# Kernel tuning notes

Hardware: AMD Instinct MI355X
Metric: run time of the kernel (lower is better)

Reference implementation:

```python
import jax, jax.numpy as jnp
import numpy as np

N_PIXELS = 262144
N_CENTERS = 1024
N_G = 256

def setup_inputs() -> dict:
    key = jax.random.key(0)
    k1, k2, k3, k4, k5 = jax.random.split(key, 5)
    return {
        "alphas": jax.random.normal(k1, (N_CENTERS, 1), dtype=jnp.float32),
        "betas": jax.random.normal(k2, (N_G, 2), dtype=jnp.float32) * 0.1,
        "K": jax.random.normal(k3, (N_PIXELS, N_G), dtype=jnp.float32) * 0.05,
        "all_pixels": jax.random.normal(k4, (N_PIXELS, 2), dtype=jnp.float32),
        "all_p_centers": jax.random.normal(k5, (N_CENTERS, 2), dtype=jnp.float32),
        "sdp2": jnp.ones((), dtype=jnp.float32) * 2.0,
    }

def reference(alphas, betas, K, all_pixels, all_p_centers, sdp2):
    # deformed pixel coordinates: (n_pixels, 2)
    deformed = all_pixels - K @ betas
    # pairwise squared distances via norm expansion (same math as the torch
    # ones-matmul broadcasting, expressed with plain broadcasting):
    p_norm2 = jnp.sum(jnp.square(deformed), axis=1, keepdims=True)      # (n_pixels, 1)
    c_norm2 = jnp.sum(jnp.square(all_p_centers), axis=1)                # (n_centers,)
    p_dot_c = 2.0 * (deformed @ all_p_centers.T)                        # (n_pixels, n_centers)
    big_matrix = p_norm2 + c_norm2[None, :] - p_dot_c
    kBp = jnp.exp(-big_matrix / (2.0 * sdp2))
    return kBp @ alphas                                                  # (n_pixels, 1)
```

## Files before the change

kernel.cpp:

```cpp
#include <hip/hip_runtime.h>

#if defined(__has_builtin)
#  if __has_builtin(__builtin_amdgcn_exp2f)
#    define EXP2F(x) __builtin_amdgcn_exp2f(x)
#  else
#    define EXP2F(x) exp2f(x)
#  endif
#else
#  define EXP2F(x) exp2f(x)
#endif

constexpr int NPIX  = 262144;
constexpr int NC    = 1024;
constexpr int NG    = 256;
constexpr int BLOCK = 256;
constexpr int GRID  = NPIX / 512;

template <int CTRL>
__device__ __forceinline__ float dpp_add(float v) {
    union { float f; int i; } u, t;
    u.f = v;
    t.i = __builtin_amdgcn_update_dpp(0, u.i, CTRL, 0xF, 0xF, true);
    return v + t.f;
}
template <int CTRL>
__device__ __forceinline__ float dpp_mov(float v) {
    union { float f; int i; } u, t;
    u.f = v;
    t.i = __builtin_amdgcn_update_dpp(0, u.i, CTRL, 0xF, 0xF, true);
    return t.f;
}
__device__ __forceinline__ float sum64_lane63(float v) {
    v = dpp_add<0xB1>(v);
    v = dpp_add<0x4E>(v);
    v = dpp_add<0x141>(v);
    v = dpp_add<0x140>(v);
    v = dpp_add<0x142>(v);
    v = dpp_add<0x143>(v);
    return v;
}
__device__ __forceinline__ float readlane63(float v) {
    union { float f; int i; } u; u.f = v;
    union { int i; float f; } r;
    r.i = __builtin_amdgcn_readlane(u.i, 63);
    return r.f;
}

__global__ __launch_bounds__(BLOCK, 4)
void kbpa_pipe(const float* __restrict__ alphas,
               const float* __restrict__ betas,
               const float* __restrict__ K,
               const float* __restrict__ pixels,
               const float* __restrict__ centers,
               const float* __restrict__ sdp2p,
               float* __restrict__ out)
{
    const int lane = threadIdx.x & 63;
    const int wave = threadIdx.x >> 6;

    const float f   = -1.44269504088896340736f / (2.0f * sdp2p[0]);
    const float m2f = -2.0f * f;

    float4 rcx[4], rcy[4], rca[4];
    {
        const float4* c4 = (const float4*)centers;
        const float4* a4 = (const float4*)alphas;
        #pragma unroll
        for (int j = 0; j < 4; ++j) {
            const float4 p0 = c4[lane * 8 + 2 * j];
            const float4 p1 = c4[lane * 8 + 2 * j + 1];
            rcx[j] = make_float4(p0.x, p0.z, p1.x, p1.z);
            rcy[j] = make_float4(p0.y, p0.w, p1.y, p1.w);
            const float4 al = a4[lane * 4 + j];
            rca[j].x = al.x * EXP2F(f * (rcx[j].x * rcx[j].x + rcy[j].x * rcy[j].x));
            rca[j].y = al.y * EXP2F(f * (rcx[j].y * rcx[j].y + rcy[j].y * rcy[j].y));
            rca[j].z = al.z * EXP2F(f * (rcx[j].z * rcx[j].z + rcy[j].z * rcy[j].z));
            rca[j].w = al.w * EXP2F(f * (rcx[j].w * rcx[j].w + rcy[j].w * rcy[j].w));
        }
    }

    const float4* bf4 = (const float4*)betas;
    const float4 bb0 = bf4[2 * lane];
    const float4 bb1 = bf4[2 * lane + 1];

    const int w0 = blockIdx.x * 512 + wave * 128;
    const float2 px0 = ((const float2*)pixels)[w0 + lane];
    const float2 px1 = ((const float2*)pixels)[w0 + 64 + lane];

    float dx0 = 0.f, dy0 = 0.f;
    #pragma unroll 1
    for (int g = 0; g < 16; ++g) {
        float4 kv[4];
        #pragma unroll
        for (int j = 0; j < 4; ++j)
            kv[j] = ((const float4*)(K + (size_t)(w0 + g * 4 + j) * NG))[lane];
        #pragma unroll
        for (int j = 0; j < 4; ++j) {
            float sx = kv[j].x * bb0.x + kv[j].y * bb0.z;
            float sy = kv[j].x * bb0.y + kv[j].y * bb0.w;
            sx = fmaf(kv[j].z, bb1.x, sx); sy = fmaf(kv[j].z, bb1.y, sy);
            sx = fmaf(kv[j].w, bb1.z, sx); sy = fmaf(kv[j].w, bb1.w, sy);
            sx = sum64_lane63(sx); sy = sum64_lane63(sy);
            const float tx = readlane63(sx);
            const float ty = readlane63(sy);
            if (lane == g * 4 + j) { dx0 = px0.x - tx; dy0 = px0.y - ty; }
        }
    }

    float dxs = m2f * dx0, dys = m2f * dy0, acc = 0.f;
    float dx1 = 0.f, dy1 = 0.f;
    #pragma unroll 1
    for (int g = 0; g < 16; ++g) {
        float4 kv[4];
        #pragma unroll
        for (int j = 0; j < 4; ++j)
            kv[j] = ((const float4*)(K + (size_t)(w0 + 64 + g * 4 + j) * NG))[lane];

        #pragma unroll
        for (int t = 0; t < 4; ++t) {
            float t0 = 0.f, t1 = 0.f, t2 = 0.f, t3 = 0.f;
            #pragma unroll
            for (int j = 0; j < 4; ++j) {
                t0 = fmaf(rca[j].x, EXP2F(fmaf(dxs, rcx[j].x, dys * rcy[j].x)), t0);
                t1 = fmaf(rca[j].y, EXP2F(fmaf(dxs, rcx[j].y, dys * rcy[j].y)), t1);
                t2 = fmaf(rca[j].z, EXP2F(fmaf(dxs, rcx[j].z, dys * rcy[j].z)), t2);
                t3 = fmaf(rca[j].w, EXP2F(fmaf(dxs, rcx[j].w, dys * rcy[j].w)), t3);
            }
            acc += (t0 + t1) + (t2 + t3);
            dxs = dpp_mov<0x121>(dxs);
            dys = dpp_mov<0x121>(dys);
            acc = dpp_mov<0x121>(acc);
        }
        if ((g & 3) == 3) {
            const int sw = lane ^ (((g >> 2) & 1) ? 32 : 16);
            dxs = __shfl(dxs, sw);
            dys = __shfl(dys, sw);
            acc = __shfl(acc, sw);
        }

        #pragma unroll
        for (int j = 0; j < 4; ++j) {
            float sx = kv[j].x * bb0.x + kv[j].y * bb0.z;
            float sy = kv[j].x * bb0.y + kv[j].y * bb0.w;
            sx = fmaf(kv[j].z, bb1.x, sx); sy = fmaf(kv[j].z, bb1.y, sy);
            sx = fmaf(kv[j].w, bb1.z, sx); sy = fmaf(kv[j].w, bb1.w, sy);
            sx = sum64_lane63(sx); sy = sum64_lane63(sy);
            const float tx = readlane63(sx);
            const float ty = readlane63(sy);
            if (lane == g * 4 + j) { dx1 = px1.x - tx; dy1 = px1.y - ty; }
        }
    }
    out[w0 + lane] = acc * EXP2F(f * (dx0 * dx0 + dy0 * dy0));

    float dxs1 = m2f * dx1, dys1 = m2f * dy1, acc1 = 0.f;
    #pragma unroll 1
    for (int round = 0; round < 4; ++round) {
        #pragma unroll 2
        for (int t = 0; t < 16; ++t) {
            float t0 = 0.f, t1 = 0.f, t2 = 0.f, t3 = 0.f;
            #pragma unroll
            for (int j = 0; j < 4; ++j) {
                t0 = fmaf(rca[j].x, EXP2F(fmaf(dxs1, rcx[j].x, dys1 * rcy[j].x)), t0);
                t1 = fmaf(rca[j].y, EXP2F(fmaf(dxs1, rcx[j].y, dys1 * rcy[j].y)), t1);
                t2 = fmaf(rca[j].z, EXP2F(fmaf(dxs1, rcx[j].z, dys1 * rcy[j].z)), t2);
                t3 = fmaf(rca[j].w, EXP2F(fmaf(dxs1, rcx[j].w, dys1 * rcy[j].w)), t3);
            }
            acc1 += (t0 + t1) + (t2 + t3);
            dxs1 = dpp_mov<0x121>(dxs1);
            dys1 = dpp_mov<0x121>(dys1);
            acc1 = dpp_mov<0x121>(acc1);
        }
        const int sw = lane ^ ((round & 1) ? 32 : 16);
        dxs1 = __shfl(dxs1, sw);
        dys1 = __shfl(dys1, sw);
        acc1 = __shfl(acc1, sw);
    }
    out[w0 + 64 + lane] = acc1 * EXP2F(f * (dx1 * dx1 + dy1 * dy1));
}

extern "C" void kernel_launch(void* const* d_in, const int* in_sizes, int n_in,
                              void* d_out, int out_size, void* d_ws, size_t ws_size,
                              hipStream_t stream)
{
    const float* alphas  = (const float*)d_in[0];
    const float* betas   = (const float*)d_in[1];
    const float* K       = (const float*)d_in[2];
    const float* pixels  = (const float*)d_in[3];
    const float* centers = (const float*)d_in[4];
    const float* sdp2    = (const float*)d_in[5];
    float* outp          = (float*)d_out;

    hipLaunchKernelGGL(kbpa_pipe, dim3(GRID), dim3(BLOCK), 0, stream,
                       alphas, betas, K, pixels, centers, sdp2, outp);
}
```

Measured before the change: 76.94 us.

## Double-buffer K row loads and remap block order across XCDs

K rows are now loaded into two alternating register buffers, so the next group's global loads are in flight while the current group is being reduced and while the exp-sum steps run. This hides memory latency in both the deformation pass and the pipelined compute pass. Block indices are remapped so that contiguous chunks of pixels go to the same group of blocks (likely per XCD), and launch bounds are relaxed to 2 waves per SIMD to give the extra buffers register room. The costs are higher register pressure and possibly lower occupancy.

Measured after the change: 72.44 us. 5.8% less time.

```diff
diff --git a/kernel.cpp b/kernel.cpp
--- a/kernel.cpp
+++ b/kernel.cpp
@@ -46,7 +46,42 @@
     return r.f;
 }
 
-__global__ __launch_bounds__(BLOCK, 4)
+#define LOAD4(BUF, ABSROW)                                                   \
+    _Pragma("unroll")                                                        \
+    for (int j = 0; j < 4; ++j)                                              \
+        BUF[j] = ((const float4*)(K + (size_t)((ABSROW) + j) * NG))[lane];
+
+#define RED4(BUF, REL, PX, DXO, DYO)                                         \
+    _Pragma("unroll")                                                        \
+    for (int j = 0; j < 4; ++j) {                                            \
+        float sx = BUF[j].x * bb0.x + BUF[j].y * bb0.z;                      \
+        float sy = BUF[j].x * bb0.y + BUF[j].y * bb0.w;                      \
+        sx = fmaf(BUF[j].z, bb1.x, sx); sy = fmaf(BUF[j].z, bb1.y, sy);      \
+        sx = fmaf(BUF[j].w, bb1.z, sx); sy = fmaf(BUF[j].w, bb1.w, sy);      \
+        sx = sum64_lane63(sx); sy = sum64_lane63(sy);                        \
+        const float tx = readlane63(sx);                                     \
+        const float ty = readlane63(sy);                                     \
+        if (lane == (REL) + j) { DXO = PX.x - tx; DYO = PX.y - ty; }         \
+    }
+
+#define BSTEPS(N)                                                            \
+    _Pragma("unroll")                                                        \
+    for (int t = 0; t < (N); ++t) {                                          \
+        float t0 = 0.f, t1 = 0.f, t2 = 0.f, t3 = 0.f;                        \
+        _Pragma("unroll")                                                    \
+        for (int j = 0; j < 4; ++j) {                                        \
+            t0 = fmaf(rca[j].x, EXP2F(fmaf(dxs, rcx[j].x, dys * rcy[j].x)), t0); \
+            t1 = fmaf(rca[j].y, EXP2F(fmaf(dxs, rcx[j].y, dys * rcy[j].y)), t1); \
+            t2 = fmaf(rca[j].z, EXP2F(fmaf(dxs, rcx[j].z, dys * rcy[j].z)), t2); \
+            t3 = fmaf(rca[j].w, EXP2F(fmaf(dxs, rcx[j].w, dys * rcy[j].w)), t3); \
+        }                                                                    \
+        acc += (t0 + t1) + (t2 + t3);                                        \
+        dxs = dpp_mov<0x121>(dxs);                            \
+        dys = dpp_mov<0x121>(dys);                                           \
+        acc = dpp_mov<0x121>(acc);                                           \
+    }
+
+__global__ __launch_bounds__(BLOCK, 2)
 void kbpa_pipe(const float* __restrict__ alphas,
                const float* __restrict__ betas,
                const float* __restrict__ K,
@@ -57,6 +92,9 @@
 {
     const int lane = threadIdx.x & 63;
     const int wave = threadIdx.x >> 6;
+
+    const int cpx = GRID / 8;
+    const int bid = (blockIdx.x & 7) * cpx + (blockIdx.x >> 3);
 
     const float f   = -1.44269504088896340736f / (2.0f * sdp2p[0]);
     const float m2f = -2.0f * f;
@@ -83,99 +121,54 @@
     const float4 bb0 = bf4[2 * lane];
     const float4 bb1 = bf4[2 * lane + 1];
 
-    const int w0 = blockIdx.x * 512 + wave * 128;
+    const int w0 = bid * 512 + wave * 128;
+    const int w1 = w0 + 64;
     const float2 px0 = ((const float2*)pixels)[w0 + lane];
-    const float2 px1 = ((const float2*)pixels)[w0 + 64 + lane];
+    const float2 px1 = ((const float2*)pixels)[w1 + lane];
 
-    float dx0 = 0.f, dy0 = 0.f;
+    float dx0 = 0.f, dy0 = 0.f, dx1 = 0.f, dy1 = 0.f;
+    float4 kva[4], kvb[4];
+
+    LOAD4(kva, w0 + 0)
     #pragma unroll 1
-    for (int g = 0; g < 16; ++g) {
-        float4 kv[4];
-        #pragma unroll
-        for (int j = 0; j < 4; ++j)
-            kv[j] = ((const float4*)(K + (size_t)(w0 + g * 4 + j) * NG))[lane];
-        #pragma unroll
-        for (int j = 0; j < 4; ++j) {
-            float sx = kv[j].x * bb0.x + kv[j].y * bb0.z;
-            float sy = kv[j].x * bb0.y + kv[j].y * bb0.w;
-            sx = fmaf(kv[j].z, bb1.x, sx); sy = fmaf(kv[j].z, bb1.y, sy);
-            sx = fmaf(kv[j].w, bb1.z, sx); sy = fmaf(kv[j].w, bb1.w, sy);
-            sx = sum64_lane63(sx); sy = sum64_lane63(sy);
-            const float tx = readlane63(sx);
-            const float ty = readlane63(sy);
-            if (lane == g * 4 + j) { dx0 = px0.x - tx; dy0 = px0.y - ty; }
-        }
+    for (int gg = 0; gg < 8; ++gg) {
+        const int g = 2 * gg;
+        LOAD4(kvb, w0 + (g + 1) * 4)
+        RED4(kva, g * 4, px0, dx0, dy0)
+        if (gg < 7) { LOAD4(kva, w0 + (g + 2) * 4) }
+        RED4(kvb, (g + 1) * 4, px0, dx0, dy0)
     }
 
     float dxs = m2f * dx0, dys = m2f * dy0, acc = 0.f;
-    float dx1 = 0.f, dy1 = 0.f;
+    LOAD4(kva, w1 + 0)
     #pragma unroll 1
-    for (int g = 0; g < 16; ++g) {
-        float4 kv[4];
-        #pragma unroll
-        for (int j = 0; j < 4; ++j)
-            kv[j] = ((const float4*)(K + (size_t)(w0 + 64 + g * 4 + j) * NG))[lane];
-
-        #pragma unroll
-        for (int t = 0; t < 4; ++t) {
-            float t0 = 0.f, t1 = 0.f, t2 = 0.f, t3 = 0.f;
-            #pragma unroll
-            for (int j = 0; j < 4; ++j) {
-                t0 = fmaf(rca[j].x, EXP2F(fmaf(dxs, rcx[j].x, dys * rcy[j].x)), t0);
-                t1 = fmaf(rca[j].y, EXP2F(fmaf(dxs, rcx[j].y, dys * rcy[j].y)), t1);
-                t2 = fmaf(rca[j].z, EXP2F(fmaf(dxs, rcx[j].z, dys * rcy[j].z)), t2);
-                t3 = fmaf(rca[j].w, EXP2F(fmaf(dxs, rcx[j].w, dys * rcy[j].w)), t3);
-            }
-            acc += (t0 + t1) + (t2 + t3);
-            dxs = dpp_mov<0x121>(dxs);
-            dys = dpp_mov<0x121>(dys);
-            acc = dpp_mov<0x121>(acc);
-        }
-        if ((g & 3) == 3) {
-            const int sw = lane ^ (((g >> 2) & 1) ? 32 : 16);
+    for (int gg = 0; gg < 8; ++gg) {
+        const int g = 2 * gg;
+        LOAD4(kvb, w1 + (g + 1) * 4)
+        BSTEPS(4)
+        RED4(kva, g * 4, px1, dx1, dy1)
+        if (gg < 7) { LOAD4(kva, w1 + (g + 2) * 4) }
+        BSTEPS(4)
+        RED4(kvb, (g + 1) * 4, px1, dx1, dy1)
+        if (gg & 1) {
+            const int sw = lane ^ ((gg & 2) ? 32 : 16);
             dxs = __shfl(dxs, sw);
             dys = __shfl(dys, sw);
             acc = __shfl(acc, sw);
         }
-
-        #pragma unroll
-        for (int j = 0; j < 4; ++j) {
-            float sx = kv[j].x * bb0.x + kv[j].y * bb0.z;
-            float sy = kv[j].x * bb0.y + kv[j].y * bb0.w;
-            sx = fmaf(kv[j].z, bb1.x, sx); sy = fmaf(kv[j].z, bb1.y, sy);
-            sx = fmaf(kv[j].w, bb1.z, sx); sy = fmaf(kv[j].w, bb1.w, sy);
-            sx = sum64_lane63(sx); sy = sum64_lane63(sy);
-            const float tx = readlane63(sx);
-            const float ty = readlane63(sy);
-            if (lane == g * 4 + j) { dx1 = px1.x - tx; dy1 = px1.y - ty; }
-        }
     }
     out[w0 + lane] = acc * EXP2F(f * (dx0 * dx0 + dy0 * dy0));
 
-    float dxs1 = m2f * dx1, dys1 = m2f * dy1, acc1 = 0.f;
+    dxs = m2f * dx1; dys = m2f * dy1; acc = 0.f;
     #pragma unroll 1
     for (int round = 0; round < 4; ++round) {
-        #pragma unroll 2
-        for (int t = 0; t < 16; ++t) {
-            float t0 = 0.f, t1 = 0.f, t2 = 0.f, t3 = 0.f;
-            #pragma unroll
-            for (int j = 0; j < 4; ++j) {
-                t0 = fmaf(rca[j].x, EXP2F(fmaf(dxs1, rcx[j].x, dys1 * rcy[j].x)), t0);
-                t1 = fmaf(rca[j].y, EXP2F(fmaf(dxs1, rcx[j].y, dys1 * rcy[j].y)), t1);
-                t2 = fmaf(rca[j].z, EXP2F(fmaf(dxs1, rcx[j].z, dys1 * rcy[j].z)), t2);
-                t3 = fmaf(rca[j].w, EXP2F(fmaf(dxs1, rcx[j].w, dys1 * rcy[j].w)), t3);
-            }
-            acc1 += (t0 + t1) + (t2 + t3);
-            dxs1 = dpp_mov<0x121>(dxs1);
-            dys1 = dpp_mov<0x121>(dys1);
-            acc1 = dpp_mov<0x121>(acc1);
-        }
+        BSTEPS(16)
         const int sw = lane ^ ((round & 1) ? 32 : 16);
-        dxs1 = __shfl(dxs1, sw);
-        dys1 = __shfl(dys1, sw);
-        acc1 = __shfl(acc1, sw);
+        dxs = __shfl(dxs, sw);
+        dys = __shfl(dys, sw);
+        acc = __shfl(acc, sw);
     }
-    out[w0 + 64 + lane] = acc1 * EXP2F(f * (dx1 * dx1 + dy1 * dy1));
+    out[w1 + lane] = acc * EXP2F(f * (dx1 * dx1 + dy1 * dy1));
 }
 
 extern "C" void kernel_launch(void* const* d_in, const int* in_sizes, int n_in,
```
